# Kernel optimization log

Measured on AMD Instinct MI355X. Metric: run time of the kernel, lower is better.

The kernel has to match this reference:

```python
import jax, jax.numpy as jnp
import numpy as np

B, T, C, H = 2, 2048, 1024, 16  # batch, seq, d_model, heads
D = C // H                       # head dim = 64


def setup_inputs() -> dict:
    key = jax.random.key(0)
    ks = jax.random.split(key, 5)
    s = 0.02  # init scale for weights
    return {
        "x": jax.random.normal(ks[0], (B, T, C), jnp.float32),
        "Wq": jax.random.normal(ks[1], (C, C), jnp.float32) * s,
        "bq": jnp.zeros((C,), jnp.float32),
        "Wk": jax.random.normal(ks[2], (C, C), jnp.float32) * s,
        "bk": jnp.zeros((C,), jnp.float32),
        "Wv": jax.random.normal(ks[3], (C, C), jnp.float32) * s,
        "bv": jnp.zeros((C,), jnp.float32),
        "Wo": jax.random.normal(ks[4], (C, C), jnp.float32) * s,
        "bo": jnp.zeros((C,), jnp.float32),
    }


def reference(x, Wq, bq, Wk, bk, Wv, bv, Wo, bo):
    b, t, c = x.shape
    h, d = H, C // H
    # QKV projections (torch Linear: x @ W.T + b), split into heads: b h t d
    q = (x @ Wq.T + bq).reshape(b, t, h, d).transpose(0, 2, 1, 3)
    k = (x @ Wk.T + bk).reshape(b, t, h, d).transpose(0, 2, 1, 3)
    v = (x @ Wv.T + bv).reshape(b, t, h, d).transpose(0, 2, 1, 3)

    scale = 1.0 / float(np.sqrt(d))
    att = jnp.einsum("bhqd,bhkd->bhqk", q, k) * scale  # [B,H,T,T]
    causal = jnp.tril(jnp.ones((t, t), dtype=bool))
    att = jnp.where(causal[None, None, :, :], att, -jnp.inf)
    att = jax.nn.softmax(att, axis=-1)
    att_weights = att  # attn_dropout with p=0 is identity

    y = jnp.einsum("bhqk,bhkd->bhqd", att, v)          # [B,H,T,D]
    y = y.transpose(0, 2, 1, 3).reshape(b, t, c)        # b q (h d)
    y = y @ Wo.T + bo                                   # out proj; resid_dropout p=0
    return y, att_weights
```

## Files before the change

kernel.cpp:

```cpp
#include <hip/hip_runtime.h>

#define DI __device__ __forceinline__

typedef __attribute__((ext_vector_type(8))) short short8;
typedef __attribute__((ext_vector_type(4))) float floatx4;
typedef unsigned short u16;

#define Bb 2
#define Tt 2048
#define Cc 1024
#define Hh 16
#define Dd 64
#define C1 0.1803368801111244f
#define NEGBIG (-1e30f)

DI float bf2f(u16 u) { union { unsigned int i; float f; } v; v.i = ((unsigned int)u) << 16; return v.f; }
DI u16 f2bf(float f) {
  union { float f; unsigned int i; } v; v.f = f;
  unsigned int i = v.i;
  unsigned int r = i + 0x7fffu + ((i >> 16) & 1u);
  return (u16)(r >> 16);
}

DI floatx4 mfma16(short8 a, short8 b, floatx4 c) {
  return __builtin_amdgcn_mfma_f32_16x16x32_bf16(a, b, c, 0, 0, 0);
}

DI void gload16(const u16* g, u16* l) {
  __builtin_amdgcn_global_load_lds(
      (const __attribute__((address_space(1))) unsigned int*)(g),
      (__attribute__((address_space(3))) unsigned int*)(l), 16, 0, 0);
}

DI uint4 load8(const void* p, size_t eoff, int isbf) {
  if (isbf) {
    return *(const uint4*)((const u16*)p + eoff);
  } else {
    const float* f = (const float*)p + eoff;
    float4 a = *(const float4*)f;
    float4 b = *(const float4*)(f + 4);
    union { uint4 u; u16 s[8]; } r;
    r.s[0] = f2bf(a.x); r.s[1] = f2bf(a.y); r.s[2] = f2bf(a.z); r.s[3] = f2bf(a.w);
    r.s[4] = f2bf(b.x); r.s[5] = f2bf(b.y); r.s[6] = f2bf(b.z); r.s[7] = f2bf(b.w);
    return r.u;
  }
}

DI float loadb(const void* p, int i, int isbf) {
  return isbf ? bf2f(((const u16*)p)[i]) : ((const float*)p)[i];
}

__global__ void detect_dtype(const u16* __restrict__ x, int* __restrict__ flag) {
  __shared__ int cnt[256];
  int c = 0;
  for (int i = threadIdx.x; i < 4096; i += 256) {
    unsigned u = x[2 * i];
    unsigned e = (u >> 7) & 0xFFu;
    c += (e == 0u || (e >= 100u && e <= 150u)) ? 1 : 0;
  }
  cnt[threadIdx.x] = c;
  __syncthreads();
  for (int s = 128; s > 0; s >>= 1) {
    if ((int)threadIdx.x < s) cnt[threadIdx.x] += cnt[threadIdx.x + s];
    __syncthreads();
  }
  if (threadIdx.x == 0) *flag = (cnt[0] > 2458) ? 1 : 0;
}

__global__ __launch_bounds__(256) void convert_all(
    const void* __restrict__ x,
    const void* __restrict__ wq, const void* __restrict__ wk,
    const void* __restrict__ wv, const void* __restrict__ wo,
    u16* __restrict__ xb,
    u16* __restrict__ wqb, u16* __restrict__ wkb,
    u16* __restrict__ wvb, u16* __restrict__ wob,
    const int* __restrict__ flagp) {
  const int isbf = *flagp;
  const void* src;
  u16* dst;
  size_t n;
  switch (blockIdx.y) {
    case 0: src = x;  dst = xb;  n = (size_t)Bb * Tt * Cc; break;
    case 1: src = wq; dst = wqb; n = (size_t)Cc * Cc; break;
    case 2: src = wk; dst = wkb; n = (size_t)Cc * Cc; break;
    case 3: src = wv; dst = wvb; n = (size_t)Cc * Cc; break;
    default: src = wo; dst = wob; n = (size_t)Cc * Cc; break;
  }
  size_t i8 = ((size_t)blockIdx.x * 256 + threadIdx.x) * 8;
  size_t step = (size_t)gridDim.x * 256 * 8;
  for (; i8 < n; i8 += step) {
    uint4 v = load8(src, i8, isbf);
    *(uint4*)(dst + i8) = v;
  }
}

__global__ __launch_bounds__(256) void qkv_gemm(
    const u16* __restrict__ Xb,
    const u16* __restrict__ Wqb, const u16* __restrict__ Wkb, const u16* __restrict__ Wvb,
    const void* __restrict__ bq, const void* __restrict__ bk, const void* __restrict__ bv,
    u16* __restrict__ Qb, u16* __restrict__ Kb, u16* __restrict__ Vb,
    const int* __restrict__ flagp) {
  __shared__ __align__(16) u16 As[128 * 32];
  __shared__ __align__(16) u16 Bs[128 * 32];
  const int isbf = *flagp;
  const int z = blockIdx.z;
  const u16* W = (z == 0) ? Wqb : (z == 1) ? Wkb : Wvb;
  const void* bias = (z == 0) ? bq : (z == 1) ? bk : bv;
  u16* Out = (z == 0) ? Qb : (z == 1) ? Kb : Vb;

  const int m0 = blockIdx.y * 128, n0 = blockIdx.x * 128;
  const int tid = threadIdx.x;
  const int w = tid >> 6, lane = tid & 63, quad = lane >> 4, l15 = lane & 15;
  const int wm = w >> 1, wn = w & 1;

  floatx4 acc[4][4];
#pragma unroll
  for (int a = 0; a < 4; ++a)
#pragma unroll
    for (int b2 = 0; b2 < 4; ++b2) acc[a][b2] = (floatx4){0.f, 0.f, 0.f, 0.f};

  const int s0 = w * 128 + lane, s1 = s0 + 64;
  const int rA0 = s0 >> 2, c0 = (s0 & 3) * 8;
  const int rA1 = s1 >> 2, c1 = (s1 & 3) * 8;
  const u16* gA0 = Xb + (size_t)(m0 + rA0) * Cc + c0;
  const u16* gA1 = Xb + (size_t)(m0 + rA1) * Cc + c1;
  const u16* gB0 = W + (size_t)(n0 + rA0) * Cc + c0;
  const u16* gB1 = W + (size_t)(n0 + rA1) * Cc + c1;
  u16* lA0 = As + w * 1024;
  u16* lA1 = As + w * 1024 + 512;
  u16* lB0 = Bs + w * 1024;
  u16* lB1 = Bs + w * 1024 + 512;

  for (int k0 = 0; k0 < Cc; k0 += 32) {
    __syncthreads();
    gload16(gA0 + k0, lA0);
    gload16(gA1 + k0, lA1);
    gload16(gB0 + k0, lB0);
    gload16(gB1 + k0, lB1);
    __syncthreads();
    short8 af[4], bfv[4];
#pragma unroll
    for (int t = 0; t < 4; ++t)
      af[t] = *(const short8*)(As + (wm * 64 + t * 16 + l15) * 32 + quad * 8);
#pragma unroll
    for (int t = 0; t < 4; ++t)
      bfv[t] = *(const short8*)(Bs + (wn * 64 + t * 16 + l15) * 32 + quad * 8);
#pragma unroll
    for (int tm = 0; tm < 4; ++tm)
#pragma unroll
      for (int tn = 0; tn < 4; ++tn) acc[tm][tn] = mfma16(af[tm], bfv[tn], acc[tm][tn]);
  }

  float bb[4];
#pragma unroll
  for (int tn = 0; tn < 4; ++tn) bb[tn] = loadb(bias, n0 + wn * 64 + tn * 16 + l15, isbf);
#pragma unroll
  for (int tm = 0; tm < 4; ++tm) {
#pragma unroll
    for (int tn = 0; tn < 4; ++tn) {
      int n = n0 + wn * 64 + tn * 16 + l15;
      int h = n >> 6, d = n & 63;
#pragma unroll
      for (int r = 0; r < 4; ++r) {
        int m = m0 + wm * 64 + tm * 16 + quad * 4 + r;
        int b = m >> 11, t = m & 2047;
        Out[(((size_t)(b * Hh + h) * Tt) + t) * Dd + d] = f2bf(acc[tm][tn][r] + bb[tn]);
      }
    }
  }
}

__global__ __launch_bounds__(256) void out_gemm(
    const u16* __restrict__ Y, const u16* __restrict__ Wob, const void* __restrict__ bo,
    float* __restrict__ Out, const int* __restrict__ flagp) {
  __shared__ __align__(16) u16 As[128 * 32];
  __shared__ __align__(16) u16 Bs[128 * 32];
  const int isbf = *flagp;
  const int m0 = blockIdx.y * 128, n0 = blockIdx.x * 128;
  const int tid = threadIdx.x;
  const int w = tid >> 6, lane = tid & 63, quad = lane >> 4, l15 = lane & 15;
  const int wm = w >> 1, wn = w & 1;

  floatx4 acc[4][4];
#pragma unroll
  for (int a = 0; a < 4; ++a)
#pragma unroll
    for (int b2 = 0; b2 < 4; ++b2) acc[a][b2] = (floatx4){0.f, 0.f, 0.f, 0.f};

  const int s0 = w * 128 + lane, s1 = s0 + 64;
  const int rA0 = s0 >> 2, c0 = (s0 & 3) * 8;
  const int rA1 = s1 >> 2, c1 = (s1 & 3) * 8;
  const u16* gA0 = Y + (size_t)(m0 + rA0) * Cc + c0;
  const u16* gA1 = Y + (size_t)(m0 + rA1) * Cc + c1;
  const u16* gB0 = Wob + (size_t)(n0 + rA0) * Cc + c0;
  const u16* gB1 = Wob + (size_t)(n0 + rA1) * Cc + c1;
  u16* lA0 = As + w * 1024;
  u16* lA1 = As + w * 1024 + 512;
  u16* lB0 = Bs + w * 1024;
  u16* lB1 = Bs + w * 1024 + 512;

  for (int k0 = 0; k0 < Cc; k0 += 32) {
    __syncthreads();
    gload16(gA0 + k0, lA0);
    gload16(gA1 + k0, lA1);
    gload16(gB0 + k0, lB0);
    gload16(gB1 + k0, lB1);
    __syncthreads();
    short8 af[4], bfv[4];
#pragma unroll
    for (int t = 0; t < 4; ++t)
      af[t] = *(const short8*)(As + (wm * 64 + t * 16 + l15) * 32 + quad * 8);
#pragma unroll
    for (int t = 0; t < 4; ++t)
      bfv[t] = *(const short8*)(Bs + (wn * 64 + t * 16 + l15) * 32 + quad * 8);
#pragma unroll
    for (int tm = 0; tm < 4; ++tm)
#pragma unroll
      for (int tn = 0; tn < 4; ++tn) acc[tm][tn] = mfma16(af[tm], bfv[tn], acc[tm][tn]);
  }

  float bb[4];
#pragma unroll
  for (int tn = 0; tn < 4; ++tn) bb[tn] = loadb(bo, n0 + wn * 64 + tn * 16 + l15, isbf);
#pragma unroll
  for (int tm = 0; tm < 4; ++tm)
#pragma unroll
    for (int tn = 0; tn < 4; ++tn) {
      int n = n0 + wn * 64 + tn * 16 + l15;
#pragma unroll
      for (int r = 0; r < 4; ++r) {
        int m = m0 + wm * 64 + tm * 16 + quad * 4 + r;
        Out[(size_t)m * Cc + n] = acc[tm][tn][r] + bb[tn];
      }
    }
}

__global__ __launch_bounds__(512) void attn_kernel(
    const u16* __restrict__ Qbuf, const u16* __restrict__ Kbuf, const u16* __restrict__ Vbuf,
    float* __restrict__ Att, u16* __restrict__ Ybuf) {
  __shared__ __align__(16) u16 Ks[128 * 72];
  __shared__ __align__(16) u16 Vts[64 * 136];
  __shared__ __align__(16) u16 Ps[8 * 16 * 40];

  const int id = blockIdx.x;
  const int zp = id >> 5;
  const int hb = id & 31;
  const int b = hb >> 4, h = hb & 15;

  const int tid = threadIdx.x;
  const int w = tid >> 6, lane = tid & 63, quad = lane >> 4, l15 = lane & 15;

  const size_t headoff = (size_t)(b * Hh + h) * Tt * Dd;
  const u16* Qh = Qbuf + headoff;
  const u16* Kh = Kbuf + headoff;
  const u16* Vh = Vbuf + headoff;
  float* attO = Att + (size_t)(b * Hh + h) * Tt * Tt;
  u16* Psw = Ps + w * 640;

  for (int half = 0; half < 2; ++half) {
    const int qt = half ? (15 - zp) : zp;
    const int q0 = qt * 128;
    const int qw = q0 + w * 16;

    short8 aq0 = *(const short8*)(Qh + (size_t)(qw + l15) * Dd + quad * 8);
    short8 aq1 = *(const short8*)(Qh + (size_t)(qw + l15) * Dd + 32 + quad * 8);

    float m4[4], l4[4];
#pragma unroll
    for (int r = 0; r < 4; ++r) { m4[r] = NEGBIG; l4[r] = 0.f; }

    for (int c = 0; c <= qt; ++c) {
      const int kb = c * 128;
      __syncthreads();
#pragma unroll
      for (int i = 0; i < 2; ++i) {
        int slot = tid + i * 512;
        int rr = slot >> 3, g = slot & 7;
        *(uint4*)(Ks + rr * 72 + g * 8) = *(const uint4*)(Kh + (size_t)(kb + rr) * Dd + g * 8);
      }
      __syncthreads();

      floatx4 s[8];
#pragma unroll
      for (int kt = 0; kt < 8; ++kt) {
        short8 b0 = *(const short8*)(Ks + (kt * 16 + l15) * 72 + quad * 8);
        short8 b1 = *(const short8*)(Ks + (kt * 16 + l15) * 72 + 32 + quad * 8);
        floatx4 t = (floatx4){0.f, 0.f, 0.f, 0.f};
        t = mfma16(aq0, b0, t);
        t = mfma16(aq1, b1, t);
        s[kt] = t;
      }

      const bool partial = (kb + 127 > qw);
#pragma unroll
      for (int r = 0; r < 4; ++r) {
        const int qi = qw + quad * 4 + r;
        float e[8];
        float bm = NEGBIG;
#pragma unroll
        for (int kt = 0; kt < 8; ++kt) {
          float s2 = s[kt][r] * C1;
          if (partial) {
            int key = kb + kt * 16 + l15;
            s2 = (key <= qi) ? s2 : NEGBIG;
          }
          e[kt] = s2;
          bm = fmaxf(bm, s2);
        }
#pragma unroll
        for (int off = 8; off >= 1; off >>= 1) bm = fmaxf(bm, __shfl_xor(bm, off, 64));
        const float mn = fmaxf(m4[r], bm);
        float sum = 0.f;
#pragma unroll
        for (int kt = 0; kt < 8; ++kt) sum += exp2f(e[kt] - mn);
#pragma unroll
        for (int off = 8; off >= 1; off >>= 1) sum += __shfl_xor(sum, off, 64);
        l4[r] = l4[r] * exp2f(m4[r] - mn) + sum;
        m4[r] = mn;
      }
    }

    float lrec[4];
#pragma unroll
    for (int r = 0; r < 4; ++r) lrec[r] = 1.0f / l4[r];

    floatx4 yacc[4];
#pragma unroll
    for (int dt = 0; dt < 4; ++dt) yacc[dt] = (floatx4){0.f, 0.f, 0.f, 0.f};

    for (int c = 0; c < Tt / 128; ++c) {
      const int kb = c * 128;
      if (c > qt) {
        uint4 z; z.x = 0u; z.y = 0u; z.z = 0u; z.w = 0u;
#pragma unroll
        for (int i = 0; i < 8; ++i) {
          int slot = tid + i * 512;
          int row = slot >> 5, g = slot & 31;
          *(uint4*)(attO + (size_t)(q0 + row) * Tt + kb + g * 4) = z;
        }
        continue;
      }
      __syncthreads();
#pragma unroll
      for (int i = 0; i < 2; ++i) {
        int slot = tid + i * 512;
        int rr = slot >> 3, g = slot & 7;
        *(uint4*)(Ks + rr * 72 + g * 8) = *(const uint4*)(Kh + (size_t)(kb + rr) * Dd + g * 8);
      }
      {
        int vrow = tid >> 2, vcb = (tid & 3) * 16;
        const u16* src = Vh + (size_t)(kb + vrow) * Dd + vcb;
        union { uint4 u; u16 sv[8]; } cv;
#pragma unroll
        for (int g = 0; g < 2; ++g) {
          cv.u = *(const uint4*)(src + g * 8);
#pragma unroll
          for (int j = 0; j < 8; ++j) Vts[(vcb + g * 8 + j) * 136 + vrow] = cv.sv[j];
        }
      }
      __syncthreads();

      floatx4 s[8];
#pragma unroll
      for (int kt = 0; kt < 8; ++kt) {
        short8 b0 = *(const short8*)(Ks + (kt * 16 + l15) * 72 + quad * 8);
        short8 b1 = *(const short8*)(Ks + (kt * 16 + l15) * 72 + 32 + quad * 8);
        floatx4 t = (floatx4){0.f, 0.f, 0.f, 0.f};
        t = mfma16(aq0, b0, t);
        t = mfma16(aq1, b1, t);
        s[kt] = t;
      }

      const bool partial = (kb + 127 > qw);
#pragma unroll
      for (int ks = 0; ks < 4; ++ks) {
#pragma unroll
        for (int kk = 0; kk < 2; ++kk) {
          const int kt = ks * 2 + kk;
#pragma unroll
          for (int r = 0; r < 4; ++r) {
            const int row = quad * 4 + r;
            const int qi = qw + row;
            const int key = kb + kt * 16 + l15;
            float p = exp2f(s[kt][r] * C1 - m4[r]) * lrec[r];
            if (partial && key > qi) p = 0.f;
            attO[(size_t)qi * Tt + key] = p;
            Psw[row * 40 + kk * 16 + l15] = f2bf(p);
          }
        }
        short8 ap = *(const short8*)(Psw + l15 * 40 + quad * 8);
#pragma unroll
        for (int dt = 0; dt < 4; ++dt) {
          short8 bv = *(const short8*)(Vts + (dt * 16 + l15) * 136 + ks * 32 + quad * 8);
          yacc[dt] = mfma16(ap, bv, yacc[dt]);
        }
      }
    }

#pragma unroll
    for (int dt = 0; dt < 4; ++dt) {
#pragma unroll
      for (int r = 0; r < 4; ++r) {
        const int qi = qw + quad * 4 + r;
        Ybuf[(size_t)(b * Tt + qi) * Cc + h * Dd + dt * 16 + l15] = f2bf(yacc[dt][r]);
      }
    }
  }
}

extern "C" void kernel_launch(void* const* d_in, const int* in_sizes, int n_in,
                              void* d_out, int out_size, void* d_ws, size_t ws_size,
                              hipStream_t stream) {
  const void* x  = d_in[0];
  const void* Wq = d_in[1];
  const void* bq = d_in[2];
  const void* Wk = d_in[3];
  const void* bk = d_in[4];
  const void* Wv = d_in[5];
  const void* bv = d_in[6];
  const void* Wo = d_in[7];
  const void* bo = d_in[8];
  float* out = (float*)d_out;

  const size_t NTC = (size_t)Bb * Tt * Cc;
  const size_t CC = (size_t)Cc * Cc;

  char* wsb = (char*)d_ws;
  int* flag = (int*)wsb;
  u16* Qb = (u16*)(wsb + 256);
  u16* Kb = Qb + NTC;
  u16* Vb = Kb + NTC;
  u16* Yb = Vb + NTC;
  u16* Xb = Yb + NTC;
  u16* Wqb = Xb + NTC;
  u16* Wkb = Wqb + CC;
  u16* Wvb = Wkb + CC;
  u16* Wob = Wvb + CC;

  hipLaunchKernelGGL(detect_dtype, dim3(1), dim3(256), 0, stream, (const u16*)x, flag);
  hipLaunchKernelGGL(convert_all, dim3(512, 5), dim3(256), 0, stream,
                     x, Wq, Wk, Wv, Wo, Xb, Wqb, Wkb, Wvb, Wob, flag);
  hipLaunchKernelGGL(qkv_gemm, dim3(8, 32, 3), dim3(256), 0, stream,
                     Xb, Wqb, Wkb, Wvb, bq, bk, bv, Qb, Kb, Vb, flag);
  float* attOut = out + NTC;
  hipLaunchKernelGGL(attn_kernel, dim3(256), dim3(512), 0, stream,
                     Qb, Kb, Vb, attOut, Yb);
  hipLaunchKernelGGL(out_gemm, dim3(8, 32, 1), dim3(256), 0, stream,
                     Yb, Wob, bo, out, flag);
}
```

Measured before the change: 709.7 us.

## Read K from global directly, double-buffer V, defer softmax reductions

The attention kernel stops staging K in shared memory and loads MFMA operands for K straight from global memory. V tiles go into a double-buffered shared array, with the next tile prefetched into registers, so each chunk needs one barrier instead of two. The per-chunk cross-lane max/sum shuffles in the statistics pass are replaced by one merge of per-lane running max and sum after the loop. Zero-filling of the masked region moves after the main loop, and exp is clamped at zero since per-lane maxima can differ. Direct global K loads may cost more bandwidth and latency than the shared-memory staging did.

```diff
diff --git a/kernel.cpp b/kernel.cpp
--- a/kernel.cpp
+++ b/kernel.cpp
@@ -238,8 +238,7 @@
 __global__ __launch_bounds__(512) void attn_kernel(
     const u16* __restrict__ Qbuf, const u16* __restrict__ Kbuf, const u16* __restrict__ Vbuf,
     float* __restrict__ Att, u16* __restrict__ Ybuf) {
-  __shared__ __align__(16) u16 Ks[128 * 72];
-  __shared__ __align__(16) u16 Vts[64 * 136];
+  __shared__ __align__(16) u16 Vts[2][64 * 136];
   __shared__ __align__(16) u16 Ps[8 * 16 * 40];
 
   const int id = blockIdx.x;
@@ -257,6 +256,9 @@
   float* attO = Att + (size_t)(b * Hh + h) * Tt * Tt;
   u16* Psw = Ps + w * 640;
 
+  const u16* Kl = Kh + (size_t)l15 * Dd + quad * 8;
+  const int vrow = tid >> 2, vcb = (tid & 3) * 16;
+
   for (int half = 0; half < 2; ++half) {
     const int qt = half ? (15 - zp) : zp;
     const int q0 = qt * 128;
@@ -271,26 +273,17 @@
 
     for (int c = 0; c <= qt; ++c) {
       const int kb = c * 128;
-      __syncthreads();
-#pragma unroll
-      for (int i = 0; i < 2; ++i) {
-        int slot = tid + i * 512;
-        int rr = slot >> 3, g = slot & 7;
-        *(uint4*)(Ks + rr * 72 + g * 8) = *(const uint4*)(Kh + (size_t)(kb + rr) * Dd + g * 8);
-      }
-      __syncthreads();
-
       floatx4 s[8];
 #pragma unroll
       for (int kt = 0; kt < 8; ++kt) {
-        short8 b0 = *(const short8*)(Ks + (kt * 16 + l15) * 72 + quad * 8);
-        short8 b1 = *(const short8*)(Ks + (kt * 16 + l15) * 72 + 32 + quad * 8);
+        const u16* kp = Kl + (size_t)(kb + kt * 16) * Dd;
+        short8 b0 = *(const short8*)(kp);
+        short8 b1 = *(const short8*)(kp + 32);
         floatx4 t = (floatx4){0.f, 0.f, 0.f, 0.f};
         t = mfma16(aq0, b0, t);
         t = mfma16(aq1, b1, t);
         s[kt] = t;
       }
-
       const bool partial = (kb + 127 > qw);
 #pragma unroll
       for (int r = 0; r < 4; ++r) {
@@ -307,19 +300,27 @@
           e[kt] = s2;
           bm = fmaxf(bm, s2);
         }
-#pragma unroll
-        for (int off = 8; off >= 1; off >>= 1) bm = fmaxf(bm, __shfl_xor(bm, off, 64));
-        const float mn = fmaxf(m4[r], bm);
+        float mn = fmaxf(m4[r], bm);
         float sum = 0.f;
 #pragma unroll
         for (int kt = 0; kt < 8; ++kt) sum += exp2f(e[kt] - mn);
-#pragma unroll
-        for (int off = 8; off >= 1; off >>= 1) sum += __shfl_xor(sum, off, 64);
         l4[r] = l4[r] * exp2f(m4[r] - mn) + sum;
         m4[r] = mn;
       }
     }
-
+#pragma unroll
+    for (int r = 0; r < 4; ++r) {
+      float m = m4[r], l = l4[r];
+#pragma unroll
+      for (int off = 1; off <= 8; off <<= 1) {
+        float mo = __shfl_xor(m, off, 64);
+        float lo = __shfl_xor(l, off, 64);
+        float mn = fmaxf(m, mo);
+        l = l * exp2f(m - mn) + lo * exp2f(mo - mn);
+        m = mn;
+      }
+      m4[r] = m; l4[r] = l;
+    }
     float lrec[4];
 #pragma unroll
     for (int r = 0; r < 4; ++r) lrec[r] = 1.0f / l4[r];
@@ -328,49 +329,40 @@
 #pragma unroll
     for (int dt = 0; dt < 4; ++dt) yacc[dt] = (floatx4){0.f, 0.f, 0.f, 0.f};
 
-    for (int c = 0; c < Tt / 128; ++c) {
+    uint4 va = *(const uint4*)(Vh + (size_t)vrow * Dd + vcb);
+    uint4 vb = *(const uint4*)(Vh + (size_t)vrow * Dd + vcb + 8);
+
+    for (int c = 0; c <= qt; ++c) {
       const int kb = c * 128;
-      if (c > qt) {
-        uint4 z; z.x = 0u; z.y = 0u; z.z = 0u; z.w = 0u;
-#pragma unroll
-        for (int i = 0; i < 8; ++i) {
-          int slot = tid + i * 512;
-          int row = slot >> 5, g = slot & 31;
-          *(uint4*)(attO + (size_t)(q0 + row) * Tt + kb + g * 4) = z;
-        }
-        continue;
-      }
-      __syncthreads();
-#pragma unroll
-      for (int i = 0; i < 2; ++i) {
-        int slot = tid + i * 512;
-        int rr = slot >> 3, g = slot & 7;
-        *(uint4*)(Ks + rr * 72 + g * 8) = *(const uint4*)(Kh + (size_t)(kb + rr) * Dd + g * 8);
-      }
+      u16* Vt = &Vts[c & 1][0];
       {
-        int vrow = tid >> 2, vcb = (tid & 3) * 16;
-        const u16* src = Vh + (size_t)(kb + vrow) * Dd + vcb;
         union { uint4 u; u16 sv[8]; } cv;
-#pragma unroll
-        for (int g = 0; g < 2; ++g) {
-          cv.u = *(const uint4*)(src + g * 8);
-#pragma unroll
-          for (int j = 0; j < 8; ++j) Vts[(vcb + g * 8 + j) * 136 + vrow] = cv.sv[j];
-        }
-      }
-      __syncthreads();
+        cv.u = va;
+#pragma unroll
+        for (int j = 0; j < 8; ++j) Vt[(vcb + j) * 136 + vrow] = cv.sv[j];
+        cv.u = vb;
+#pragma unroll
+        for (int j = 0; j < 8; ++j) Vt[(vcb + 8 + j) * 136 + vrow] = cv.sv[j];
+      }
+      if (c < qt) {
+        va = *(const uint4*)(Vh + (size_t)(kb + 128 + vrow) * Dd + vcb);
+        vb = *(const uint4*)(Vh + (size_t)(kb + 128 + vrow) * Dd + vcb + 8);
+      }
 
       floatx4 s[8];
 #pragma unroll
       for (int kt = 0; kt < 8; ++kt) {
-        short8 b0 = *(const short8*)(Ks + (kt * 16 + l15) * 72 + quad * 8);
-        short8 b1 = *(const short8*)(Ks + (kt * 16 + l15) * 72 + 32 + quad * 8);
+        const u16* kp = Kl + (size_t)(kb + kt * 16) * Dd;
+        short8 b0 = *(const short8*)(kp);
+        short8 b1 = *(const short8*)(kp + 32);
         floatx4 t = (floatx4){0.f, 0.f, 0.f, 0.f};
         t = mfma16(aq0, b0, t);
         t = mfma16(aq1, b1, t);
         s[kt] = t;
       }
 
+      __syncthreads();
+
       const bool partial = (kb + 127 > qw);
 #pragma unroll
       for (int ks = 0; ks < 4; ++ks) {
@@ -382,7 +374,7 @@
             const int row = quad * 4 + r;
             const int qi = qw + row;
             const int key = kb + kt * 16 + l15;
-            float p = exp2f(s[kt][r] * C1 - m4[r]) * lrec[r];
+            float p = exp2f(fminf(s[kt][r] * C1 - m4[r], 0.f)) * lrec[r];
             if (partial && key > qi) p = 0.f;
             attO[(size_t)qi * Tt + key] = p;
             Psw[row * 40 + kk * 16 + l15] = f2bf(p);
@@ -391,8 +383,21 @@
         short8 ap = *(const short8*)(Psw + l15 * 40 + quad * 8);
 #pragma unroll
         for (int dt = 0; dt < 4; ++dt) {
-          short8 bv = *(const short8*)(Vts + (dt * 16 + l15) * 136 + ks * 32 + quad * 8);
+          short8 bv = *(const short8*)(Vt + (dt * 16 + l15) * 136 + ks * 32 + quad * 8);
           yacc[dt] = mfma16(ap, bv, yacc[dt]);
+        }
+      }
+    }
+
+    {
+      uint4 z; z.x = 0u; z.y = 0u; z.z = 0u; z.w = 0u;
+      for (int c = qt + 1; c < 16; ++c) {
+        const int kb = c * 128;
+#pragma unroll
+        for (int i = 0; i < 8; ++i) {
+          int slot = tid + i * 512;
+          int row = slot >> 5, g = slot & 31;
+          *(uint4*)(attO + (size_t)(q0 + row) * Tt + kb + g * 4) = z;
         }
       }
     }
```

Measured after the change: 751.7 us. 5.9% more time.
